# Optimization experiments

Measured on AMD Instinct MI355X. Metric: run time of the kernel, lower is better.

The kernel has to match this reference:

```python
import jax, jax.numpy as jnp
import numpy as np

HIDDEN = 1024
HEADS = 16
HEAD = HIDDEN // HEADS


def setup_inputs() -> dict:
    key = jax.random.key(0)
    ks = jax.random.split(key, 10)
    B, T, N = 4, 1024, 1024
    x = jax.random.normal(ks[0], (B, T, HIDDEN), dtype=jnp.float32)
    encoder_feature = jax.random.normal(ks[1], (B, N, HIDDEN), dtype=jnp.float32)
    s = 1.0 / np.sqrt(HIDDEN)
    Wq = jax.random.normal(ks[2], (HIDDEN, HIDDEN), dtype=jnp.float32) * s
    bq = jax.random.normal(ks[3], (HIDDEN,), dtype=jnp.float32) * 0.02
    Wk = jax.random.normal(ks[4], (HIDDEN, HIDDEN), dtype=jnp.float32) * s
    bk = jax.random.normal(ks[5], (HIDDEN,), dtype=jnp.float32) * 0.02
    Wv = jax.random.normal(ks[6], (HIDDEN, HIDDEN), dtype=jnp.float32) * s
    bv = jax.random.normal(ks[7], (HIDDEN,), dtype=jnp.float32) * 0.02
    return {"x": x, "encoder_feature": encoder_feature,
            "Wq": Wq, "bq": bq, "Wk": Wk, "bk": bk, "Wv": Wv, "bv": bv}


def reference(x, encoder_feature, Wq, bq, Wk, bk, Wv, bv):
    B, T, _ = x.shape
    N = encoder_feature.shape[1]
    # torch Linear: y = x @ W.T + b
    q = (x @ Wq.T + bq).reshape(B, T, HEADS, HEAD)
    k = (encoder_feature @ Wk.T + bk).reshape(B, N, HEADS, HEAD)
    v = (encoder_feature @ Wv.T + bv).reshape(B, N, HEADS, HEAD)
    att = jnp.einsum('bthd,bnhd->bhtn', q, k) / jnp.sqrt(jnp.float32(HEAD))
    # causal tril mask sliced to (T, N): position t attends to n <= t
    mask = jnp.tril(jnp.ones((T, N), dtype=bool))
    att = jnp.where(mask[None, None], att, jnp.finfo(att.dtype).min)
    att = jax.nn.softmax(att, axis=-1)
    out = jnp.einsum('bhtn,bnhd->bthd', att, v).reshape(B, T, HIDDEN)
    # NOTE: original forward never applies out_proj; dropout=0.0 (identity)
    return out
```

## Files before the change

kernel.cpp:

```cpp
#include <hip/hip_runtime.h>
#include <hip/hip_bf16.h>
#include <cstdint>
#include <cstddef>

#define B_SZ 4
#define T_SZ 1024
#define N_SZ 1024
#define HID 1024
#define NHEADS 16
#define DHEAD 64

typedef __bf16 bf16x8 __attribute__((ext_vector_type(8)));
typedef __bf16 bf16x4 __attribute__((ext_vector_type(4)));
typedef float floatx4 __attribute__((ext_vector_type(4)));

#define LDT 72
#define LKV 72
#define LP  72

#define SM_SCALE_LOG2E 0.18033688011112042f

__device__ __forceinline__ void async_copy16(const void* gsrc, void* ldst) {
    __builtin_amdgcn_global_load_lds(
        (const __attribute__((address_space(1))) void*)(uintptr_t)gsrc,
        (__attribute__((address_space(3))) void*)(uintptr_t)ldst, 16, 0, 0);
}

__global__ __launch_bounds__(256)
void cvt5_f32_bf16(const float* __restrict__ x, const float* __restrict__ enc,
                   const float* __restrict__ wq, const float* __restrict__ wk,
                   const float* __restrict__ wv,
                   __bf16* __restrict__ xb, __bf16* __restrict__ eb,
                   __bf16* __restrict__ wqb, __bf16* __restrict__ wkb,
                   __bf16* __restrict__ wvb)
{
    const int bx = blockIdx.x;
    const float* s; __bf16* d; int base;
    if (bx < 2048)      { s = x;   d = xb;  base = bx; }
    else if (bx < 4096) { s = enc; d = eb;  base = bx - 2048; }
    else if (bx < 4608) { s = wq;  d = wqb; base = bx - 4096; }
    else if (bx < 5120) { s = wk;  d = wkb; base = bx - 4608; }
    else                { s = wv;  d = wvb; base = bx - 5120; }
    const size_t off = (size_t)base * 2048 + (size_t)threadIdx.x * 8;
    const float4 a = *(const float4*)(s + off);
    const float4 b = *(const float4*)(s + off + 4);
    bf16x8 o;
    o[0] = (__bf16)a.x; o[1] = (__bf16)a.y; o[2] = (__bf16)a.z; o[3] = (__bf16)a.w;
    o[4] = (__bf16)b.x; o[5] = (__bf16)b.y; o[6] = (__bf16)b.z; o[7] = (__bf16)b.w;
    *(bf16x8*)(d + off) = o;
}

__global__ __launch_bounds__(256)
void gemm3_bt_bias(const __bf16* __restrict__ xb, const __bf16* __restrict__ eb,
                   const __bf16* __restrict__ wqb, const __bf16* __restrict__ wkb,
                   const __bf16* __restrict__ wvb,
                   const float* __restrict__ bq, const float* __restrict__ bk,
                   const float* __restrict__ bv,
                   __bf16* __restrict__ qo, __bf16* __restrict__ ko,
                   __bf16* __restrict__ vo)
{
    constexpr int K = HID;
    __shared__ __align__(16) __bf16 As[128 * 64];
    __shared__ __align__(16) __bf16 Bs[128 * 64];

    const __bf16* A; const __bf16* W; const float* bias; __bf16* C;
    if (blockIdx.z == 0)      { A = xb; W = wqb; bias = bq; C = qo; }
    else if (blockIdx.z == 1) { A = eb; W = wkb; bias = bk; C = ko; }
    else                      { A = eb; W = wvb; bias = bv; C = vo; }

    const int tid  = threadIdx.x;
    const int wave = tid >> 6;
    const int lane = tid & 63;
    const int l15  = lane & 15;
    const int quad = lane >> 4;
    const int bm = blockIdx.y * 128;
    const int bn = blockIdx.x * 128;
    const int wm = (wave >> 1) * 64;
    const int wn = (wave & 1) * 64;

    floatx4 acc[4][4];
#pragma unroll
    for (int i = 0; i < 4; ++i)
#pragma unroll
        for (int j = 0; j < 4; ++j)
            acc[i][j] = (floatx4)(0.0f);

    const int sr = tid >> 3;
    const int sc = (((tid & 7) ^ (sr & 7))) * 8;

    for (int k0 = 0; k0 < K; k0 += 64) {
#pragma unroll
        for (int p = 0; p < 4; ++p) {
            const int r = p * 32 + sr;
            async_copy16(A + (size_t)(bm + r) * K + k0 + sc,
                         (char*)As + p * 4096 + tid * 16);
            async_copy16(W + (size_t)(bn + r) * K + k0 + sc,
                         (char*)Bs + p * 4096 + tid * 16);
        }
        __syncthreads();
#pragma unroll
        for (int kk = 0; kk < 2; ++kk) {
            const int ch = kk * 4 + quad;
            bf16x8 af[4], bfr[4];
#pragma unroll
            for (int i = 0; i < 4; ++i) {
                const int ra = wm + i * 16 + l15;
                const int rb = wn + i * 16 + l15;
                af[i]  = *(const bf16x8*)((const char*)As + ra * 128 + ((ch ^ (ra & 7)) << 4));
                bfr[i] = *(const bf16x8*)((const char*)Bs + rb * 128 + ((ch ^ (rb & 7)) << 4));
            }
#pragma unroll
            for (int mi = 0; mi < 4; ++mi)
#pragma unroll
                for (int ni = 0; ni < 4; ++ni)
                    acc[mi][ni] = __builtin_amdgcn_mfma_f32_16x16x32_bf16(
                        af[mi], bfr[ni], acc[mi][ni], 0, 0, 0);
        }
        __syncthreads();
    }

    const int crow0 = bm + wm + quad * 4;
    const int ccol0 = bn + wn + l15;
#pragma unroll
    for (int ni = 0; ni < 4; ++ni) {
        const int n = ccol0 + ni * 16;
        const float bias_f = bias[n];
#pragma unroll
        for (int mi = 0; mi < 4; ++mi) {
#pragma unroll
            for (int r = 0; r < 4; ++r) {
                const int m = crow0 + mi * 16 + r;
                C[(size_t)m * HID + n] = (__bf16)(acc[mi][ni][r] + bias_f);
            }
        }
    }
}

__global__ __launch_bounds__(256)
void gemm_bt_bias_f32in(const float* __restrict__ A,
                        const float* __restrict__ W,
                        const float* __restrict__ bias,
                        __hip_bfloat16* __restrict__ C)
{
    constexpr int K = HID;
    __shared__ __align__(16) __hip_bfloat16 As[128 * LDT];
    __shared__ __align__(16) __hip_bfloat16 Bs[128 * LDT];

    const int tid  = threadIdx.x;
    const int wave = tid >> 6;
    const int lane = tid & 63;
    const int bm = blockIdx.y * 128;
    const int bn = blockIdx.x * 128;
    const int wm = (wave >> 1) * 64;
    const int wn = (wave & 1) * 64;

    floatx4 acc[4][4];
#pragma unroll
    for (int i = 0; i < 4; ++i)
#pragma unroll
        for (int j = 0; j < 4; ++j)
            acc[i][j] = (floatx4)(0.0f);

    const int lr = tid >> 4;
    const int lc = (tid & 15) * 4;

    for (int k0 = 0; k0 < K; k0 += 64) {
#pragma unroll
        for (int qq = 0; qq < 8; ++qq) {
            const int r = lr + qq * 16;
            const float4 a4 = *(const float4*)(A + (size_t)(bm + r) * K + k0 + lc);
            const float4 w4 = *(const float4*)(W + (size_t)(bn + r) * K + k0 + lc);
            bf16x4 av, wv;
            av[0] = (__bf16)a4.x; av[1] = (__bf16)a4.y; av[2] = (__bf16)a4.z; av[3] = (__bf16)a4.w;
            wv[0] = (__bf16)w4.x; wv[1] = (__bf16)w4.y; wv[2] = (__bf16)w4.z; wv[3] = (__bf16)w4.w;
            *(bf16x4*)(As + r * LDT + lc) = av;
            *(bf16x4*)(Bs + r * LDT + lc) = wv;
        }
        __syncthreads();
#pragma unroll
        for (int kk = 0; kk < 2; ++kk) {
            const int krow = kk * 32 + (lane >> 4) * 8;
            const int mrow = wm + (lane & 15);
            const int nrow = wn + (lane & 15);
            bf16x8 af[4], bfr[4];
#pragma unroll
            for (int i = 0; i < 4; ++i) {
                af[i]  = *(const bf16x8*)(As + (mrow + i * 16) * LDT + krow);
                bfr[i] = *(const bf16x8*)(Bs + (nrow + i * 16) * LDT + krow);
            }
#pragma unroll
            for (int mi = 0; mi < 4; ++mi)
#pragma unroll
                for (int ni = 0; ni < 4; ++ni)
                    acc[mi][ni] = __builtin_amdgcn_mfma_f32_16x16x32_bf16(
                        af[mi], bfr[ni], acc[mi][ni], 0, 0, 0);
        }
        __syncthreads();
    }

    const int crow0 = bm + wm + (lane >> 4) * 4;
    const int ccol0 = bn + wn + (lane & 15);
#pragma unroll
    for (int ni = 0; ni < 4; ++ni) {
        const int n = ccol0 + ni * 16;
        const float bias_f = bias[n];
#pragma unroll
        for (int mi = 0; mi < 4; ++mi) {
#pragma unroll
            for (int r = 0; r < 4; ++r) {
                const int m = crow0 + mi * 16 + r;
                C[(size_t)m * HID + n] = __float2bfloat16(acc[mi][ni][r] + bias_f);
            }
        }
    }
}

__global__ __launch_bounds__(256)
void attn_flash_mfma_v4(const __bf16* __restrict__ q,
                        const __bf16* __restrict__ k,
                        const __bf16* __restrict__ v,
                        float* __restrict__ out)
{
    __shared__ __align__(16) __bf16 Ks[2][64 * LKV];
    __shared__ __align__(16) __bf16 Vt[2][64 * LKV];
    __shared__ __align__(16) __bf16 Ps[4][32 * LP];

    const int tid  = threadIdx.x;
    const int wave = tid >> 6;
    const int lane = tid & 63;
    const int l15  = lane & 15;
    const int quad = lane >> 4;

    const int bx = blockIdx.x;
    const int jj = bx & 7;
    const int bt = ((bx >> 8) & 1) ? jj : 7 - jj;
    const int bh = bx >> 3;
    const int h  = bh & (NHEADS - 1);
    const int b  = bh >> 4;
    const int t0 = bt * 128;

    const __bf16* kbase = k + (size_t)b * N_SZ * HID + h * DHEAD;
    const __bf16* vbase = v + (size_t)b * N_SZ * HID + h * DHEAD;

    bf16x8 qf[2][2];
    {
        const __bf16* qb = q + (size_t)(b * T_SZ + t0 + wave * 32) * HID + h * DHEAD;
#pragma unroll
        for (int g = 0; g < 2; ++g)
#pragma unroll
            for (int kk = 0; kk < 2; ++kk) {
                const bf16x8 raw = *(const bf16x8*)(qb + (size_t)(g * 16 + l15) * HID
                                                    + kk * 32 + quad * 8);
#pragma unroll
                for (int j = 0; j < 8; ++j)
                    qf[g][kk][j] = (__bf16)((float)raw[j] * SM_SCALE_LOG2E);
            }
    }

    const int kr = tid >> 3;
    const int kc = (tid & 7) * 8;
    const int vn = tid & 63;
    const int vd = (tid >> 6) * 8;

#pragma unroll
    for (int p = 0; p < 2; ++p) {
        *(bf16x8*)(&Ks[0][(kr + p * 32) * LKV + kc]) =
            *(const bf16x8*)(kbase + (size_t)(kr + p * 32) * HID + kc);
        const bf16x8 vv = *(const bf16x8*)(vbase + (size_t)vn * HID + vd + p * 32);
#pragma unroll
        for (int j = 0; j < 8; ++j)
            Vt[0][(vd + p * 32 + j) * LKV + vn] = vv[j];
    }
    __syncthreads();

    float lsum[2] = {0.f, 0.f};
    floatx4 oacc[2][4];
#pragma unroll
    for (int g = 0; g < 2; ++g)
#pragma unroll
        for (int nd = 0; nd < 4; ++nd) oacc[g][nd] = (floatx4)(0.0f);

    __bf16* pw = &Ps[wave][0];
    const int ntiles = 2 * bt + 2;

    for (int it = 0; it < ntiles; ++it) {
        const int bi = it & 1;
        const int n0 = it * 64;

        bf16x8 nk0, nk1, nv0, nv1;
        const bool pf = (it + 1 < ntiles);
        if (pf) {
            const int nn0 = n0 + 64;
            nk0 = *(const bf16x8*)(kbase + (size_t)(nn0 + kr) * HID + kc);
            nk1 = *(const bf16x8*)(kbase + (size_t)(nn0 + kr + 32) * HID + kc);
            nv0 = *(const bf16x8*)(vbase + (size_t)(nn0 + vn) * HID + vd);
            nv1 = *(const bf16x8*)(vbase + (size_t)(nn0 + vn) * HID + vd + 32);
        }

        floatx4 st[2][4];
#pragma unroll
        for (int g = 0; g < 2; ++g)
#pragma unroll
            for (int ni = 0; ni < 4; ++ni) st[g][ni] = (floatx4)(0.0f);
        const __bf16* ksb = &Ks[bi][0];
#pragma unroll
        for (int kk = 0; kk < 2; ++kk) {
            const int ko = kk * 32 + quad * 8;
#pragma unroll
            for (int ni = 0; ni < 4; ++ni) {
                const bf16x8 af = *(const bf16x8*)(ksb + (ni * 16 + l15) * LKV + ko);
                st[0][ni] = __builtin_amdgcn_mfma_f32_16x16x32_bf16(af, qf[0][kk], st[0][ni], 0, 0, 0);
                st[1][ni] = __builtin_amdgcn_mfma_f32_16x16x32_bf16(af, qf[1][kk], st[1][ni], 0, 0, 0);
            }
        }

        const bool msk = (it >= 2 * bt);
#pragma unroll
        for (int g = 0; g < 2; ++g) {
            const int tq = t0 + wave * 32 + g * 16 + l15;
#pragma unroll
            for (int ni = 0; ni < 4; ++ni) {
                bf16x4 pk;
#pragma unroll
                for (int r = 0; r < 4; ++r) {
                    float p = exp2f(st[g][ni][r]);
                    if (msk) {
                        const int nn = n0 + ni * 16 + quad * 4 + r;
                        p = (nn > tq) ? 0.f : p;
                    }
                    lsum[g] += p;
                    pk[r] = (__bf16)p;
                }
                *(bf16x4*)(pw + (g * 16 + l15) * LP + ni * 16 + quad * 4) = pk;
            }
        }


        const __bf16* vtb = &Vt[bi][0];
#pragma unroll
        for (int kk = 0; kk < 2; ++kk) {
            const int ko = kk * 32 + quad * 8;
            const bf16x8 bp0 = *(const bf16x8*)(pw + l15 * LP + ko);
            const bf16x8 bp1 = *(const bf16x8*)(pw + (16 + l15) * LP + ko);
#pragma unroll
            for (int nd = 0; nd < 4; ++nd) {
                const bf16x8 av = *(const bf16x8*)(vtb + (nd * 16 + l15) * LKV + ko);
                oacc[0][nd] = __builtin_amdgcn_mfma_f32_16x16x32_bf16(av, bp0, oacc[0][nd], 0, 0, 0);
                oacc[1][nd] = __builtin_amdgcn_mfma_f32_16x16x32_bf16(av, bp1, oacc[1][nd], 0, 0, 0);
            }
        }

        if (pf) {
            const int wb = bi ^ 1;
            *(bf16x8*)(&Ks[wb][kr * LKV + kc]) = nk0;
            *(bf16x8*)(&Ks[wb][(kr + 32) * LKV + kc]) = nk1;
#pragma unroll
            for (int j = 0; j < 8; ++j) {
                Vt[wb][(vd + j) * LKV + vn] = nv0[j];
                Vt[wb][(vd + 32 + j) * LKV + vn] = nv1[j];
            }
        }
        __syncthreads();
    }

#pragma unroll
    for (int g = 0; g < 2; ++g) {
        lsum[g] += __shfl_xor(lsum[g], 16, 64);
        lsum[g] += __shfl_xor(lsum[g], 32, 64);
    }
#pragma unroll
    for (int g = 0; g < 2; ++g) {
        const float invl = 1.0f / lsum[g];
        const int trow = t0 + wave * 32 + g * 16 + l15;
        float* ob = out + (size_t)(b * T_SZ + trow) * HID + h * DHEAD + quad * 4;
#pragma unroll
        for (int nd = 0; nd < 4; ++nd) {
            float4 o4;
            o4.x = oacc[g][nd][0] * invl;
            o4.y = oacc[g][nd][1] * invl;
            o4.z = oacc[g][nd][2] * invl;
            o4.w = oacc[g][nd][3] * invl;
            *(float4*)(ob + nd * 16) = o4;
        }
    }
}

extern "C" void kernel_launch(void* const* d_in, const int* in_sizes, int n_in,
                              void* d_out, int out_size, void* d_ws, size_t ws_size,
                              hipStream_t stream) {
    const float* x   = (const float*)d_in[0];
    const float* enc = (const float*)d_in[1];
    const float* Wq  = (const float*)d_in[2];
    const float* bq  = (const float*)d_in[3];
    const float* Wk  = (const float*)d_in[4];
    const float* bk  = (const float*)d_in[5];
    const float* Wv  = (const float*)d_in[6];
    const float* bv  = (const float*)d_in[7];
    float* out = (float*)d_out;

    char* ws = (char*)d_ws;
    const size_t MiB = 1024 * 1024;
    __bf16* q_ws = (__bf16*)(ws);
    __bf16* k_ws = (__bf16*)(ws + 8 * MiB);
    __bf16* v_ws = (__bf16*)(ws + 16 * MiB);

    const dim3 blk(256);
    if (ws_size >= 46 * MiB) {
        __bf16* xb  = (__bf16*)(ws + 24 * MiB);
        __bf16* eb  = (__bf16*)(ws + 32 * MiB);
        __bf16* wqb = (__bf16*)(ws + 40 * MiB);
        __bf16* wkb = (__bf16*)(ws + 42 * MiB);
        __bf16* wvb = (__bf16*)(ws + 44 * MiB);
        cvt5_f32_bf16<<<dim3(5632), blk, 0, stream>>>(x, enc, Wq, Wk, Wv,
                                                      xb, eb, wqb, wkb, wvb);
        gemm3_bt_bias<<<dim3(8, 32, 3), blk, 0, stream>>>(
            xb, eb, wqb, wkb, wvb, bq, bk, bv, q_ws, k_ws, v_ws);
    } else {
        const dim3 gg(HID / 128, (B_SZ * T_SZ) / 128);
        gemm_bt_bias_f32in<<<gg, blk, 0, stream>>>(x,   Wq, bq, (__hip_bfloat16*)q_ws);
        gemm_bt_bias_f32in<<<gg, blk, 0, stream>>>(enc, Wk, bk, (__hip_bfloat16*)k_ws);
        gemm_bt_bias_f32in<<<gg, blk, 0, stream>>>(enc, Wv, bv, (__hip_bfloat16*)v_ws);
    }

    attn_flash_mfma_v4<<<dim3(512), blk, 0, stream>>>(q_ws, k_ws, v_ws, out);
}
```

Before: 172.6 us.

## Fuse fp32-to-bf16 conversion into a double-buffered, register-prefetched QKV GEMM

Drops the separate conversion kernel and the bf16 staging buffers. The merged QKV GEMM now reads fp32 inputs directly, converts them in registers and writes swizzled bf16 tiles into double-buffered LDS. The next K-tile's global loads are issued before the current tile's MFMAs, which removes one kernel launch and a full extra read and write of the inputs. The trade-off is higher register pressure from the prefetch buffers, double the LDS footprint, and twice the global read bytes per tile compared with loading pre-converted bf16.

Result: slower. 200.2 us (+15.9%).

```diff
diff --git a/kernel.cpp b/kernel.cpp
--- a/kernel.cpp
+++ b/kernel.cpp
@@ -14,59 +14,28 @@
 typedef __bf16 bf16x4 __attribute__((ext_vector_type(4)));
 typedef float floatx4 __attribute__((ext_vector_type(4)));
 
-#define LDT 72
 #define LKV 72
 #define LP  72
 
 #define SM_SCALE_LOG2E 0.18033688011112042f
 
-__device__ __forceinline__ void async_copy16(const void* gsrc, void* ldst) {
-    __builtin_amdgcn_global_load_lds(
-        (const __attribute__((address_space(1))) void*)(uintptr_t)gsrc,
-        (__attribute__((address_space(3))) void*)(uintptr_t)ldst, 16, 0, 0);
-}
-
 __global__ __launch_bounds__(256)
-void cvt5_f32_bf16(const float* __restrict__ x, const float* __restrict__ enc,
-                   const float* __restrict__ wq, const float* __restrict__ wk,
-                   const float* __restrict__ wv,
-                   __bf16* __restrict__ xb, __bf16* __restrict__ eb,
-                   __bf16* __restrict__ wqb, __bf16* __restrict__ wkb,
-                   __bf16* __restrict__ wvb)
-{
-    const int bx = blockIdx.x;
-    const float* s; __bf16* d; int base;
-    if (bx < 2048)      { s = x;   d = xb;  base = bx; }
-    else if (bx < 4096) { s = enc; d = eb;  base = bx - 2048; }
-    else if (bx < 4608) { s = wq;  d = wqb; base = bx - 4096; }
-    else if (bx < 5120) { s = wk;  d = wkb; base = bx - 4608; }
-    else                { s = wv;  d = wvb; base = bx - 5120; }
-    const size_t off = (size_t)base * 2048 + (size_t)threadIdx.x * 8;
-    const float4 a = *(const float4*)(s + off);
-    const float4 b = *(const float4*)(s + off + 4);
-    bf16x8 o;
-    o[0] = (__bf16)a.x; o[1] = (__bf16)a.y; o[2] = (__bf16)a.z; o[3] = (__bf16)a.w;
-    o[4] = (__bf16)b.x; o[5] = (__bf16)b.y; o[6] = (__bf16)b.z; o[7] = (__bf16)b.w;
-    *(bf16x8*)(d + off) = o;
-}
-
-__global__ __launch_bounds__(256)
-void gemm3_bt_bias(const __bf16* __restrict__ xb, const __bf16* __restrict__ eb,
-                   const __bf16* __restrict__ wqb, const __bf16* __restrict__ wkb,
-                   const __bf16* __restrict__ wvb,
-                   const float* __restrict__ bq, const float* __restrict__ bk,
-                   const float* __restrict__ bv,
-                   __bf16* __restrict__ qo, __bf16* __restrict__ ko,
-                   __bf16* __restrict__ vo)
+void gemm3_f32_pipe(const float* __restrict__ x, const float* __restrict__ enc,
+                    const float* __restrict__ wq, const float* __restrict__ wk,
+                    const float* __restrict__ wv,
+                    const float* __restrict__ bq, const float* __restrict__ bk,
+                    const float* __restrict__ bv,
+                    __bf16* __restrict__ qo, __bf16* __restrict__ ko,
+                    __bf16* __restrict__ vo)
 {
     constexpr int K = HID;
-    __shared__ __align__(16) __bf16 As[128 * 64];
-    __shared__ __align__(16) __bf16 Bs[128 * 64];
-
-    const __bf16* A; const __bf16* W; const float* bias; __bf16* C;
-    if (blockIdx.z == 0)      { A = xb; W = wqb; bias = bq; C = qo; }
-    else if (blockIdx.z == 1) { A = eb; W = wkb; bias = bk; C = ko; }
-    else                      { A = eb; W = wvb; bias = bv; C = vo; }
+    __shared__ __align__(16) __bf16 As[2][128 * 64];
+    __shared__ __align__(16) __bf16 Bs[2][128 * 64];
+
+    const float* A; const float* W; const float* bias; __bf16* C;
+    if (blockIdx.z == 0)      { A = x;   W = wq; bias = bq; C = qo; }
+    else if (blockIdx.z == 1) { A = enc; W = wk; bias = bk; C = ko; }
+    else                      { A = enc; W = wv; bias = bv; C = vo; }
 
     const int tid  = threadIdx.x;
     const int wave = tid >> 6;
@@ -85,29 +54,56 @@
         for (int j = 0; j < 4; ++j)
             acc[i][j] = (floatx4)(0.0f);
 
-    const int sr = tid >> 3;
-    const int sc = (((tid & 7) ^ (sr & 7))) * 8;
-
-    for (int k0 = 0; k0 < K; k0 += 64) {
+    const int sr     = tid >> 3;
+    const int scol   = (tid & 7) * 8;
+    const int dchunk = (tid & 7) ^ (sr & 7);
+    const size_t arow = (size_t)(bm + sr) * K + scol;
+    const size_t wrow = (size_t)(bn + sr) * K + scol;
+
+    {
 #pragma unroll
         for (int p = 0; p < 4; ++p) {
-            const int r = p * 32 + sr;
-            async_copy16(A + (size_t)(bm + r) * K + k0 + sc,
-                         (char*)As + p * 4096 + tid * 16);
-            async_copy16(W + (size_t)(bn + r) * K + k0 + sc,
-                         (char*)Bs + p * 4096 + tid * 16);
-        }
-        __syncthreads();
+            const float4 a0 = *(const float4*)(A + arow + (size_t)p * 32 * K);
+            const float4 a1 = *(const float4*)(A + arow + (size_t)p * 32 * K + 4);
+            const float4 w0 = *(const float4*)(W + wrow + (size_t)p * 32 * K);
+            const float4 w1 = *(const float4*)(W + wrow + (size_t)p * 32 * K + 4);
+            bf16x8 av, wv8;
+            av[0] = (__bf16)a0.x; av[1] = (__bf16)a0.y; av[2] = (__bf16)a0.z; av[3] = (__bf16)a0.w;
+            av[4] = (__bf16)a1.x; av[5] = (__bf16)a1.y; av[6] = (__bf16)a1.z; av[7] = (__bf16)a1.w;
+            wv8[0] = (__bf16)w0.x; wv8[1] = (__bf16)w0.y; wv8[2] = (__bf16)w0.z; wv8[3] = (__bf16)w0.w;
+            wv8[4] = (__bf16)w1.x; wv8[5] = (__bf16)w1.y; wv8[6] = (__bf16)w1.z; wv8[7] = (__bf16)w1.w;
+            *(bf16x8*)(&As[0][(sr + p * 32) * 64 + dchunk * 8]) = av;
+            *(bf16x8*)(&Bs[0][(sr + p * 32) * 64 + dchunk * 8]) = wv8;
+        }
+    }
+    __syncthreads();
+
+    for (int it = 0; it < 16; ++it) {
+        const int bi = it & 1;
+        const bool pf = (it + 1 < 16);
+
+        float4 ra0[4], ra1[4], rw0[4], rw1[4];
+        if (pf) {
+            const int k0 = (it + 1) * 64;
+#pragma unroll
+            for (int p = 0; p < 4; ++p) {
+                ra0[p] = *(const float4*)(A + arow + (size_t)p * 32 * K + k0);
+                ra1[p] = *(const float4*)(A + arow + (size_t)p * 32 * K + k0 + 4);
+                rw0[p] = *(const float4*)(W + wrow + (size_t)p * 32 * K + k0);
+                rw1[p] = *(const float4*)(W + wrow + (size_t)p * 32 * K + k0 + 4);
+            }
+        }
+
 #pragma unroll
         for (int kk = 0; kk < 2; ++kk) {
             const int ch = kk * 4 + quad;
             bf16x8 af[4], bfr[4];
 #pragma unroll
             for (int i = 0; i < 4; ++i) {
-                const int ra = wm + i * 16 + l15;
-                const int rb = wn + i * 16 + l15;
-                af[i]  = *(const bf16x8*)((const char*)As + ra * 128 + ((ch ^ (ra & 7)) << 4));
-                bfr[i] = *(const bf16x8*)((const char*)Bs + rb * 128 + ((ch ^ (rb & 7)) << 4));
+                const int ra_ = wm + i * 16 + l15;
+                const int rb_ = wn + i * 16 + l15;
+                af[i]  = *(const bf16x8*)((const char*)&As[bi][0] + ra_ * 128 + ((ch ^ (ra_ & 7)) << 4));
+                bfr[i] = *(const bf16x8*)((const char*)&Bs[bi][0] + rb_ * 128 + ((ch ^ (rb_ & 7)) << 4));
             }
 #pragma unroll
             for (int mi = 0; mi < 4; ++mi)
@@ -116,6 +112,24 @@
                     acc[mi][ni] = __builtin_amdgcn_mfma_f32_16x16x32_bf16(
                         af[mi], bfr[ni], acc[mi][ni], 0, 0, 0);
         }
+
+        if (pf) {
+            const int wb = bi ^ 1;
+#pragma unroll
+            for (int p = 0; p < 4; ++p) {
+                bf16x8 av, wv8;
+                av[0] = (__bf16)ra0[p].x; av[1] = (__bf16)ra0[p].y;
+                av[2] = (__bf16)ra0[p].z; av[3] = (__bf16)ra0[p].w;
+                av[4] = (__bf16)ra1[p].x; av[5] = (__bf16)ra1[p].y;
+                av[6] = (__bf16)ra1[p].z; av[7] = (__bf16)ra1[p].w;
+                wv8[0] = (__bf16)rw0[p].x; wv8[1] = (__bf16)rw0[p].y;
+                wv8[2] = (__bf16)rw0[p].z; wv8[3] = (__bf16)rw0[p].w;
+                wv8[4] = (__bf16)rw1[p].x; wv8[5] = (__bf16)rw1[p].y;
+                wv8[6] = (__bf16)rw1[p].z; wv8[7] = (__bf16)rw1[p].w;
+                *(bf16x8*)(&As[wb][(sr + p * 32) * 64 + dchunk * 8]) = av;
+                *(bf16x8*)(&Bs[wb][(sr + p * 32) * 64 + dchunk * 8]) = wv8;
+            }
+        }
         __syncthreads();
     }
 
@@ -131,85 +145,6 @@
             for (int r = 0; r < 4; ++r) {
                 const int m = crow0 + mi * 16 + r;
                 C[(size_t)m * HID + n] = (__bf16)(acc[mi][ni][r] + bias_f);
-            }
-        }
-    }
-}
-
-__global__ __launch_bounds__(256)
-void gemm_bt_bias_f32in(const float* __restrict__ A,
-                        const float* __restrict__ W,
-                        const float* __restrict__ bias,
-                        __hip_bfloat16* __restrict__ C)
-{
-    constexpr int K = HID;
-    __shared__ __align__(16) __hip_bfloat16 As[128 * LDT];
-    __shared__ __align__(16) __hip_bfloat16 Bs[128 * LDT];
-
-    const int tid  = threadIdx.x;
-    const int wave = tid >> 6;
-    const int lane = tid & 63;
-    const int bm = blockIdx.y * 128;
-    const int bn = blockIdx.x * 128;
-    const int wm = (wave >> 1) * 64;
-    const int wn = (wave & 1) * 64;
-
-    floatx4 acc[4][4];
-#pragma unroll
-    for (int i = 0; i < 4; ++i)
-#pragma unroll
-        for (int j = 0; j < 4; ++j)
-            acc[i][j] = (floatx4)(0.0f);
-
-    const int lr = tid >> 4;
-    const int lc = (tid & 15) * 4;
-
-    for (int k0 = 0; k0 < K; k0 += 64) {
-#pragma unroll
-        for (int qq = 0; qq < 8; ++qq) {
-            const int r = lr + qq * 16;
-            const float4 a4 = *(const float4*)(A + (size_t)(bm + r) * K + k0 + lc);
-            const float4 w4 = *(const float4*)(W + (size_t)(bn + r) * K + k0 + lc);
-            bf16x4 av, wv;
-            av[0] = (__bf16)a4.x; av[1] = (__bf16)a4.y; av[2] = (__bf16)a4.z; av[3] = (__bf16)a4.w;
-            wv[0] = (__bf16)w4.x; wv[1] = (__bf16)w4.y; wv[2] = (__bf16)w4.z; wv[3] = (__bf16)w4.w;
-            *(bf16x4*)(As + r * LDT + lc) = av;
-            *(bf16x4*)(Bs + r * LDT + lc) = wv;
-        }
-        __syncthreads();
-#pragma unroll
-        for (int kk = 0; kk < 2; ++kk) {
-            const int krow = kk * 32 + (lane >> 4) * 8;
-            const int mrow = wm + (lane & 15);
-            const int nrow = wn + (lane & 15);
-            bf16x8 af[4], bfr[4];
-#pragma unroll
-            for (int i = 0; i < 4; ++i) {
-                af[i]  = *(const bf16x8*)(As + (mrow + i * 16) * LDT + krow);
-                bfr[i] = *(const bf16x8*)(Bs + (nrow + i * 16) * LDT + krow);
-            }
-#pragma unroll
-            for (int mi = 0; mi < 4; ++mi)
-#pragma unroll
-                for (int ni = 0; ni < 4; ++ni)
-                    acc[mi][ni] = __builtin_amdgcn_mfma_f32_16x16x32_bf16(
-                        af[mi], bfr[ni], acc[mi][ni], 0, 0, 0);
-        }
-        __syncthreads();
-    }
-
-    const int crow0 = bm + wm + (lane >> 4) * 4;
-    const int ccol0 = bn + wn + (lane & 15);
-#pragma unroll
-    for (int ni = 0; ni < 4; ++ni) {
-        const int n = ccol0 + ni * 16;
-        const float bias_f = bias[n];
-#pragma unroll
-        for (int mi = 0; mi < 4; ++mi) {
-#pragma unroll
-            for (int r = 0; r < 4; ++r) {
-                const int m = crow0 + mi * 16 + r;
-                C[(size_t)m * HID + n] = __float2bfloat16(acc[mi][ni][r] + bias_f);
             }
         }
     }
@@ -334,7 +269,6 @@
                 *(bf16x4*)(pw + (g * 16 + l15) * LP + ni * 16 + quad * 4) = pk;
             }
         }
-
 
         const __bf16* vtb = &Vt[bi][0];
 #pragma unroll
@@ -405,22 +339,8 @@
     __bf16* v_ws = (__bf16*)(ws + 16 * MiB);
 
     const dim3 blk(256);
-    if (ws_size >= 46 * MiB) {
-        __bf16* xb  = (__bf16*)(ws + 24 * MiB);
-        __bf16* eb  = (__bf16*)(ws + 32 * MiB);
-        __bf16* wqb = (__bf16*)(ws + 40 * MiB);
-        __bf16* wkb = (__bf16*)(ws + 42 * MiB);
-        __bf16* wvb = (__bf16*)(ws + 44 * MiB);
-        cvt5_f32_bf16<<<dim3(5632), blk, 0, stream>>>(x, enc, Wq, Wk, Wv,
-                                                      xb, eb, wqb, wkb, wvb);
-        gemm3_bt_bias<<<dim3(8, 32, 3), blk, 0, stream>>>(
-            xb, eb, wqb, wkb, wvb, bq, bk, bv, q_ws, k_ws, v_ws);
-    } else {
-        const dim3 gg(HID / 128, (B_SZ * T_SZ) / 128);
-        gemm_bt_bias_f32in<<<gg, blk, 0, stream>>>(x,   Wq, bq, (__hip_bfloat16*)q_ws);
-        gemm_bt_bias_f32in<<<gg, blk, 0, stream>>>(enc, Wk, bk, (__hip_bfloat16*)k_ws);
-        gemm_bt_bias_f32in<<<gg, blk, 0, stream>>>(enc, Wv, bv, (__hip_bfloat16*)v_ws);
-    }
+    gemm3_f32_pipe<<<dim3(8, 32, 3), blk, 0, stream>>>(
+        x, enc, Wq, Wk, Wv, bq, bk, bv, q_ws, k_ws, v_ws);
 
     attn_flash_mfma_v4<<<dim3(512), blk, 0, stream>>>(q_ws, k_ws, v_ws, out);
 }
```
